# Kernel optimization log

Measured on AMD Instinct MI355X. Metric: run time of the kernel, lower is better.

The kernel has to match this reference:

```python
import jax, jax.numpy as jnp
import numpy as np
import math

N_NODES, N_EDGES, NNZ, D, L = 100000, 20000, 500000, 128, 4
ALPHA, LAMDA = 0.1, 0.5


def setup_inputs() -> dict:
    key = jax.random.key(0)
    ks = jax.random.split(key, 16)
    x = jax.random.normal(ks[0], (N_NODES, D), jnp.float32)
    e = jax.random.normal(ks[1], (N_EDGES, D), jnp.float32)
    nodes = jax.random.randint(ks[2], (NNZ,), 0, N_NODES)
    edges = jnp.sort(jax.random.randint(ks[3], (NNZ,), 0, N_EDGES)).at[-1].set(N_EDGES - 1)
    hyperedge_index = jnp.stack([nodes, edges]).astype(jnp.int32)
    dist_v2e = jax.random.randint(ks[4], (NNZ,), 0, 64).astype(jnp.float32)
    deg_v2e = jax.random.randint(ks[5], (NNZ,), 0, 64).astype(jnp.float32)
    dist_e2v = jax.random.randint(ks[6], (NNZ,), 0, 64).astype(jnp.float32)
    deg_e2v = jax.random.randint(ks[7], (NNZ,), 0, 64).astype(jnp.float32)
    s = 0.05
    W0 = jax.random.normal(ks[8], (D, D), jnp.float32) * s
    b0 = jnp.zeros((D,), jnp.float32)
    Wn = jax.random.normal(ks[9], (L, D, D), jnp.float32) * s
    We = jax.random.normal(ks[10], (L, D, D), jnp.float32) * s
    attn_w = jax.random.normal(ks[11], (L, 2 * D), jnp.float32) * s
    attn_b = jnp.zeros((L,), jnp.float32)
    wd_w = jax.random.normal(ks[12], (L,), jnp.float32) * s
    wd_b = jnp.zeros((L,), jnp.float32)
    wg_w = jax.random.normal(ks[13], (L,), jnp.float32) * s
    wg_b = jnp.zeros((L,), jnp.float32)
    return dict(x=x, e=e, hyperedge_index=hyperedge_index, dist_v2e=dist_v2e,
                deg_v2e=deg_v2e, dist_e2v=dist_e2v, deg_e2v=deg_e2v,
                W0=W0, b0=b0, Wn=Wn, We=We, attn_w=attn_w, attn_b=attn_b,
                wd_w=wd_w, wd_b=wd_b, wg_w=wg_w, wg_b=wg_b)


def _seg_softmax(s, idx, num):
    # numerically-stable scatter_softmax over segments idx
    m = jax.ops.segment_max(s, idx, num_segments=num)
    ex = jnp.exp(s - m[idx])
    den = jax.ops.segment_sum(ex, idx, num_segments=num)
    return ex / den[idx]


def _forward(x, e, hei, dv2e, gv2e, de2v, ge2v, W0, b0, Wn, We, aw, ab, wdw, wdb, wgw, wgb):
    nodes, edges = hei[0], hei[1]
    N, E = x.shape[0], e.shape[0]
    ones = jnp.ones(nodes.shape[0], x.dtype)
    dV = jax.ops.segment_sum(ones, nodes, num_segments=N)
    cnt = jax.ops.segment_sum(ones, edges, num_segments=E)
    dE = jax.ops.segment_sum(dV[nodes], edges, num_segments=E) / jnp.maximum(cnt, 1.0)
    degV = jnp.where(dV > 0, dV ** -0.5, 1.0)[:, None]   # [N,1]
    degE = jnp.where(dE > 0, dE ** -0.5, 1.0)[:, None]   # [E,1]

    x = jax.nn.relu(x @ W0 + b0)
    x0, e0 = x, e
    d = x.shape[1]
    for i in range(L):
        beta = math.log(LAMDA / (i + 1) + 1.0)
        # v2e attention: concat [x[nodes], e[edges]] -> softmax over edge segments
        sx1 = x @ aw[i, :d]; se1 = e @ aw[i, d:]
        s_v2e = sx1[nodes] + se1[edges] + ab[i] + dv2e * wdw[i] + wdb[i] + gv2e * wgw[i] + wgb[i]
        a_v2e = _seg_softmax(s_v2e, edges, E)[:, None]
        # e2v attention (flipped): concat [e[edges], x[nodes]] -> softmax over node segments
        se2 = e @ aw[i, :d]; sx2 = x @ aw[i, d:]
        s_e2v = se2[edges] + sx2[nodes] + ab[i] + de2v * wdw[i] + wdb[i] + ge2v * wgw[i] + wgb[i]
        a_e2v = _seg_softmax(s_e2v, nodes, N)[:, None]

        Xe1 = jax.ops.segment_sum(x[nodes] * a_v2e, edges, num_segments=E) * degE
        Xv1 = jax.ops.segment_sum(Xe1[edges] * a_e2v, nodes, num_segments=N) * degV
        Xv2 = jax.ops.segment_sum(e[edges] * a_e2v, nodes, num_segments=N) * degV
        Xe2 = jax.ops.segment_sum(Xv2[nodes] * a_v2e, edges, num_segments=E) * degE
        xm = (Xv1 + Xv2) * 0.5
        em = (Xe1 + Xe2) * 0.5
        xi = (1 - ALPHA) * xm + ALPHA * x0
        x = (1 - beta) * xi + beta * (xi @ Wn[i])
        ei = (1 - ALPHA) * em + ALPHA * e0
        e = (1 - beta) * ei + beta * (ei @ We[i])
        if i < L - 1:
            x = jax.nn.relu(x)
            e = jax.nn.relu(e)
    return x, e


def reference(x, e, hyperedge_index, dist_v2e, deg_v2e, dist_e2v, deg_e2v,
              W0, b0, Wn, We, attn_w, attn_b, wd_w, wd_b, wg_w, wg_b):
    return _forward(x, e, hyperedge_index, dist_v2e, deg_v2e, dist_e2v, deg_e2v,
                    W0, b0, Wn, We, attn_w, attn_b, wd_w, wd_b, wg_w, wg_b)
```

## Files before the change

kernel.cpp:

```cpp
#include <hip/hip_runtime.h>
#include <hip/hip_fp16.h>
#include <math.h>

#define DD 128
#define SCAN_BLOCKS 256
#define SMAX_CAP 128

typedef _Float16 f16x8 __attribute__((ext_vector_type(8)));
typedef float f32x4 __attribute__((ext_vector_type(4)));

__device__ inline float wave_sum(float v){
#pragma unroll
  for (int m = 32; m >= 1; m >>= 1) v += __shfl_xor(v, m, 64);
  return v;
}
__device__ inline int wave_sum_i(int v){
#pragma unroll
  for (int m = 32; m >= 1; m >>= 1) v += __shfl_xor(v, m, 64);
  return v;
}


__global__ void k_edge_offsets(const int* __restrict__ edges, int nnz, int E,
                               int* __restrict__ eo){
  int e = blockIdx.x * blockDim.x + threadIdx.x;
  if (e > E) return;
  int lo = 0, hi = nnz;
  while (lo < hi){ int mid = (lo + hi) >> 1; if (edges[mid] < e) lo = mid + 1; else hi = mid; }
  eo[e] = lo;
}

__global__ void k_hist(const int* __restrict__ nodes, int nnz, int* __restrict__ dV){
  int k = blockIdx.x * blockDim.x + threadIdx.x;
  if (k < nnz) atomicAdd(&dV[nodes[k]], 1);
}

__global__ __launch_bounds__(256) void k_scan_partial(const int* __restrict__ dV, int N,
                                                      int* __restrict__ part){
  int b = blockIdx.x, t = threadIdx.x;
  int chunk = (N + SCAN_BLOCKS - 1) / SCAN_BLOCKS;
  int s0 = b * chunk, s1 = min(s0 + chunk, N);
  int sum = 0;
  for (int n = s0 + t; n < s1; n += 256) sum += dV[n];
  sum = wave_sum_i(sum);
  __shared__ int wred[4];
  int lane = t & 63, wid = t >> 6;
  if (lane == 0) wred[wid] = sum;
  __syncthreads();
  if (t == 0) part[b] = wred[0] + wred[1] + wred[2] + wred[3];
}

__global__ __launch_bounds__(SCAN_BLOCKS) void k_scan_blocksums(int* __restrict__ part){
  __shared__ int sh[SCAN_BLOCKS];
  int t = threadIdx.x;
  int v = part[t];
  sh[t] = v; __syncthreads();
  for (int off = 1; off < SCAN_BLOCKS; off <<= 1){
    int add = (t >= off) ? sh[t - off] : 0;
    __syncthreads();
    sh[t] += add;
    __syncthreads();
  }
  part[t] = sh[t] - v;
}

__global__ __launch_bounds__(256) void k_scan_apply(const int* __restrict__ dV, int N, int nnz,
    const int* __restrict__ partScan, int* __restrict__ no, int* __restrict__ nfill,
    float* __restrict__ degV){
  int b = blockIdx.x, t = threadIdx.x;
  int chunk = (N + SCAN_BLOCKS - 1) / SCAN_BLOCKS;
  int s0 = b * chunk, s1 = min(s0 + chunk, N);
  int lane = t & 63, wid = t >> 6;
  __shared__ int wtot[4];
  __shared__ int s_run;
  if (t == 0) s_run = partScan[b];
  __syncthreads();
  for (int base = s0; base < s1; base += 256){
    int n = base + t;
    int d = (n < s1) ? dV[n] : 0;
    int v = d;
#pragma unroll
    for (int off = 1; off < 64; off <<= 1){
      int o = __shfl_up(v, off, 64);
      if (lane >= off) v += o;
    }
    if (lane == 63) wtot[wid] = v;
    __syncthreads();
    int run0 = s_run;
    int woff = 0;
    for (int w = 0; w < wid; w++) woff += wtot[w];
    if (n < s1){
      int excl = run0 + woff + v - d;
      no[n] = excl; nfill[n] = excl;
      degV[n] = d > 0 ? 1.0f / sqrtf((float)d) : 1.0f;
    }
    int btot = wtot[0] + wtot[1] + wtot[2] + wtot[3];
    __syncthreads();
    if (t == 0) s_run = run0 + btot;
    __syncthreads();
  }
  if (b == 0 && t == 0) no[N] = nnz;
}

__global__ void k_perm(const int* __restrict__ nodes, int nnz,
                       int* __restrict__ nfill, int* __restrict__ perm){
  int k = blockIdx.x * blockDim.x + threadIdx.x;
  if (k < nnz){ int pos = atomicAdd(&nfill[nodes[k]], 1); perm[pos] = k; }
}

__global__ void k_pack(const int* __restrict__ perm, const int* __restrict__ edges,
                       const float* __restrict__ dist, const float* __restrict__ deg,
                       int nnz, float2* __restrict__ pack){
  int j = blockIdx.x * blockDim.x + threadIdx.x;
  if (j < nnz){
    int k = perm[j];
    pack[j] = make_float2(__int_as_float(edges[k]), dist[k] + 64.f * deg[k]);
  }
}

__global__ void k_edge_deg(const int* __restrict__ nodes, const int* __restrict__ eo, int E,
                           const int* __restrict__ dV, float* __restrict__ degE){
  int e = blockIdx.x * blockDim.x + threadIdx.x;
  if (e >= E) return;
  int b = eo[e], en = eo[e + 1];
  float s = 0.f;
  for (int k = b; k < en; k++) s += (float)dV[nodes[k]];
  float cnt = (float)(en - b);
  float dE = s / fmaxf(cnt, 1.0f);
  degE[e] = dE > 0.f ? 1.0f / sqrtf(dE) : 1.0f;
}

__global__ __launch_bounds__(256) void k_einit(const float2* __restrict__ e_in2,
    const float* __restrict__ aw1, const float* __restrict__ aw2,
    int E, __half2* __restrict__ ET, __half2* __restrict__ e0h,
    float* __restrict__ se1, float* __restrict__ se2){
  int wave = threadIdx.x >> 6, lane = threadIdx.x & 63;
  int e = blockIdx.x * 4 + wave;
  if (e >= E) return;
  float2 v = e_in2[(size_t)e * 64 + lane];
  __half2 h = __floats2half2_rn(v.x, v.y);
  ET[(size_t)e * 128 + 2 * lane + 1] = h;
  e0h[(size_t)e * 64 + lane] = h;
  float2 a2v = ((const float2*)aw2)[lane];
  float2 a1v = ((const float2*)aw1)[lane];
  float s1 = v.x * a2v.x + v.y * a2v.y;
  float s2 = v.x * a1v.x + v.y * a1v.y;
  s1 = wave_sum(s1); s2 = wave_sum(s2);
  if (lane == 0){ se1[e] = s1; se2[e] = s2; }
}

__global__ void k_wcast(const float* __restrict__ W0, const float* __restrict__ Wn,
                        const float* __restrict__ We, _Float16* __restrict__ Wt){
  int idx = blockIdx.x * 256 + threadIdx.x;
  if (idx >= 9 * 16384) return;
  int m = idx >> 14, r = idx & 16383;
  int n = r >> 7, k = r & 127;
  float v;
  if (m == 0){
    v = W0[k * 128 + n];
  } else {
    int i = (m <= 4) ? m - 1 : m - 5;
    const float* src = (m <= 4) ? Wn + (size_t)i * 16384 : We + (size_t)i * 16384;
    float beta = logf(0.5f / (float)(i + 1) + 1.0f);
    v = beta * src[k * 128 + n] + ((n == k) ? (1.0f - beta) : 0.f);
  }
  Wt[(size_t)m * 16384 + n * 128 + k] = (_Float16)v;
}


__device__ inline void acc8h(const float4 q, float w, float* a){
  float2 h0 = __half22float2(*(const __half2*)&q.x);
  float2 h1 = __half22float2(*(const __half2*)&q.y);
  float2 h2v = __half22float2(*(const __half2*)&q.z);
  float2 h3 = __half22float2(*(const __half2*)&q.w);
  a[0] += w * h0.x; a[1] += w * h0.y; a[2] += w * h1.x; a[3] += w * h1.y;
  a[4] += w * h2v.x; a[5] += w * h2v.y; a[6] += w * h3.x; a[7] += w * h3.y;
}

__global__ __launch_bounds__(256) void k_sma1(
    const int* __restrict__ nodes, const int* __restrict__ eo,
    const float* __restrict__ sx1, const float* __restrict__ se1,
    const float* __restrict__ dist, const float* __restrict__ deg,
    const float* __restrict__ ab, const float* __restrict__ wdw, const float* __restrict__ wdb,
    const float* __restrict__ wgw, const float* __restrict__ wgb, int li,
    const float* __restrict__ degE, const float4* __restrict__ xh4,
    int E, float* __restrict__ a_v2e, float* __restrict__ esc, __half2* __restrict__ ET){
  __shared__ float lw[8][SMAX_CAP];
  int l32 = threadIdx.x & 31;
  int grp = threadIdx.x >> 5;
  int e = blockIdx.x * 8 + grp;
  if (e >= E) return;
  int b = eo[e], en = eo[e + 1];
  int l16 = l32 & 15, hf = l32 >> 4;
  if (b >= en){
    if (l32 == 0) esc[e] = 0.f;
    if (hf == 0){
      __half2 z = __floats2half2_rn(0.f, 0.f);
      size_t o = (size_t)e * 128 + 8 * l16;
      ET[o] = z; ET[o + 2] = z; ET[o + 4] = z; ET[o + 6] = z;
    }
    return;
  }
  float base = se1[e] + ab[li] + wdb[li] + wgb[li];
  float wd = wdw[li], wg = wgw[li];
  float m = -INFINITY;
  float sreg[4];
#pragma unroll
  for (int c = 0; c < 4; c++){
    int k = b + l32 + 32 * c;
    if (k < en){
      float s = sx1[nodes[k]] + base + dist[k] * wd + deg[k] * wg;
      sreg[c] = s; m = fmaxf(m, s);
    }
  }
  for (int k = b + l32 + SMAX_CAP; k < en; k += 32){
    float s = sx1[nodes[k]] + base + dist[k] * wd + deg[k] * wg;
    m = fmaxf(m, s);
  }
#pragma unroll
  for (int mm = 16; mm >= 1; mm >>= 1) m = fmaxf(m, __shfl_xor(m, mm, 32));
  float sum = 0.f;
#pragma unroll
  for (int c = 0; c < 4; c++){
    int k = b + l32 + 32 * c;
    if (k < en){
      float ex = __expf(sreg[c] - m);
      a_v2e[k] = ex; lw[grp][l32 + 32 * c] = ex; sum += ex;
    }
  }
  for (int k = b + l32 + SMAX_CAP; k < en; k += 32){
    float s = sx1[nodes[k]] + base + dist[k] * wd + deg[k] * wg;
    float ex = __expf(s - m);
    a_v2e[k] = ex; sum += ex;
  }
#pragma unroll
  for (int mm = 16; mm >= 1; mm >>= 1) sum += __shfl_xor(sum, mm, 32);
  float sc = degE[e] / sum;
  if (l32 == 0) esc[e] = sc;
  float a[8] = {0.f, 0.f, 0.f, 0.f, 0.f, 0.f, 0.f, 0.f};
  int k = b + hf;
  for (; k + 2 < en; k += 4){
    int n0 = nodes[k], n1 = nodes[k + 2];
    float w0 = (k - b < SMAX_CAP) ? lw[grp][k - b] : a_v2e[k];
    float w1 = (k + 2 - b < SMAX_CAP) ? lw[grp][k + 2 - b] : a_v2e[k + 2];
    float4 v0 = xh4[(size_t)n0 * 16 + l16];
    float4 v1 = xh4[(size_t)n1 * 16 + l16];
    acc8h(v0, w0, a); acc8h(v1, w1, a);
  }
  for (; k < en; k += 2){
    int n = nodes[k];
    float w = (k - b < SMAX_CAP) ? lw[grp][k - b] : a_v2e[k];
    float4 v = xh4[(size_t)n * 16 + l16];
    acc8h(v, w, a);
  }
#pragma unroll
  for (int j = 0; j < 8; j++) a[j] += __shfl_xor(a[j], 16, 32);
  if (hf == 0){
    size_t o = (size_t)e * 128 + 8 * l16;
    ET[o]     = __floats2half2_rn(a[0] * sc, a[1] * sc);
    ET[o + 2] = __floats2half2_rn(a[2] * sc, a[3] * sc);
    ET[o + 4] = __floats2half2_rn(a[4] * sc, a[5] * sc);
    ET[o + 6] = __floats2half2_rn(a[6] * sc, a[7] * sc);
  }
}

__device__ inline void acc8(const float4 q, float w, float* a1, float* a2){
  float2 x0 = __half22float2(*(const __half2*)&q.x);
  float2 e0 = __half22float2(*(const __half2*)&q.y);
  float2 x1 = __half22float2(*(const __half2*)&q.z);
  float2 e1 = __half22float2(*(const __half2*)&q.w);
  a1[0] += w * x0.x; a1[1] += w * x0.y; a1[2] += w * x1.x; a1[3] += w * x1.y;
  a2[0] += w * e0.x; a2[1] += w * e0.y; a2[2] += w * e1.x; a2[3] += w * e1.y;
}

__global__ __launch_bounds__(256) void k_agg2f(
    const float2* __restrict__ pack, const int* __restrict__ no,
    const float* __restrict__ se2, const float* __restrict__ sx2,
    const float* __restrict__ ab, const float* __restrict__ wdw, const float* __restrict__ wdb,
    const float* __restrict__ wgw, const float* __restrict__ wgb, int li,
    const float4* __restrict__ ETq,
    const float* __restrict__ degV, const __half2* __restrict__ x0h,
    int N, __half2* __restrict__ Xv2h, __half2* __restrict__ xiH){
  int l32 = threadIdx.x & 31;
  int grp = threadIdx.x >> 5;
  int n = blockIdx.x * 8 + grp;
  if (n >= N) return;
  int b = no[n], en = no[n + 1];
  float base = sx2[n] + ab[li] + wdb[li] + wgb[li];
  float wd = wdw[li], wg = wgw[li];
  float2 x0v2 = *(const float2*)&x0h[(size_t)n * 64 + 2 * l32];
  float l_run = 0.f;
  float a1[4] = {0.f, 0.f, 0.f, 0.f}, a2[4] = {0.f, 0.f, 0.f, 0.f};
  if (en - b <= 32){
    int cs = en - b;
    float s = -INFINITY; int e_l = 0;
    if (l32 < cs){
      float2 pk = pack[b + l32];
      e_l = __float_as_int(pk.x);
      int vi = (int)pk.y;
      s = se2[e_l] + base + (float)(vi & 63) * wd + (float)(vi >> 6) * wg;
    }
    float m_c = s;
#pragma unroll
    for (int mm = 16; mm >= 1; mm >>= 1) m_c = fmaxf(m_c, __shfl_xor(m_c, mm, 32));
    float p = (l32 < cs) ? __expf(s - m_c) : 0.f;
    l_run = p;
#pragma unroll
    for (int mm = 16; mm >= 1; mm >>= 1) l_run += __shfl_xor(l_run, mm, 32);
    int jj = 0;
    for (; jj + 3 < cs; jj += 4){
      float w0 = __shfl(p, jj, 32);
      float w1 = __shfl(p, jj + 1, 32);
      float w2 = __shfl(p, jj + 2, 32);
      float w3 = __shfl(p, jj + 3, 32);
      int e0i = __shfl(e_l, jj, 32);
      int e1i = __shfl(e_l, jj + 1, 32);
      int e2i = __shfl(e_l, jj + 2, 32);
      int e3i = __shfl(e_l, jj + 3, 32);
      float4 q0 = ETq[(size_t)e0i * 32 + l32];
      float4 q1 = ETq[(size_t)e1i * 32 + l32];
      float4 q2 = ETq[(size_t)e2i * 32 + l32];
      float4 q3 = ETq[(size_t)e3i * 32 + l32];
      acc8(q0, w0, a1, a2);
      acc8(q1, w1, a1, a2);
      acc8(q2, w2, a1, a2);
      acc8(q3, w3, a1, a2);
    }
    for (; jj < cs; jj++){
      float w = __shfl(p, jj, 32);
      int ei_ = __shfl(e_l, jj, 32);
      float4 q = ETq[(size_t)ei_ * 32 + l32];
      acc8(q, w, a1, a2);
    }
  } else {
    float m_run = -INFINITY;
    for (int cb = b; cb < en; cb += 32){
      int cs = min(32, en - cb);
      float s = -INFINITY; int e_l = 0;
      if (l32 < cs){
        float2 pk = pack[cb + l32];
        e_l = __float_as_int(pk.x);
        int vi = (int)pk.y;
        s = se2[e_l] + base + (float)(vi & 63) * wd + (float)(vi >> 6) * wg;
      }
      float m_c = s;
#pragma unroll
      for (int mm = 16; mm >= 1; mm >>= 1) m_c = fmaxf(m_c, __shfl_xor(m_c, mm, 32));
      float p = (l32 < cs) ? __expf(s - m_c) : 0.f;
      float l_c = p;
#pragma unroll
      for (int mm = 16; mm >= 1; mm >>= 1) l_c += __shfl_xor(l_c, mm, 32);
      float m_new = fmaxf(m_run, m_c);
      float f_old = __expf(m_run - m_new);
      float f_c = __expf(m_c - m_new);
#pragma unroll
      for (int r = 0; r < 4; r++){ a1[r] *= f_old; a2[r] *= f_old; }
      l_run = l_run * f_old + l_c * f_c;
      m_run = m_new;
      int jj = 0;
      for (; jj + 3 < cs; jj += 4){
        float w0 = __shfl(p, jj, 32) * f_c;
        float w1 = __shfl(p, jj + 1, 32) * f_c;
        float w2 = __shfl(p, jj + 2, 32) * f_c;
        float w3 = __shfl(p, jj + 3, 32) * f_c;
        int e0i = __shfl(e_l, jj, 32);
        int e1i = __shfl(e_l, jj + 1, 32);
        int e2i = __shfl(e_l, jj + 2, 32);
        int e3i = __shfl(e_l, jj + 3, 32);
        float4 q0 = ETq[(size_t)e0i * 32 + l32];
        float4 q1 = ETq[(size_t)e1i * 32 + l32];
        float4 q2 = ETq[(size_t)e2i * 32 + l32];
        float4 q3 = ETq[(size_t)e3i * 32 + l32];
        acc8(q0, w0, a1, a2);
        acc8(q1, w1, a1, a2);
        acc8(q2, w2, a1, a2);
        acc8(q3, w3, a1, a2);
      }
      for (; jj < cs; jj++){
        float w = __shfl(p, jj, 32) * f_c;
        int ei_ = __shfl(e_l, jj, 32);
        float4 q = ETq[(size_t)ei_ * 32 + l32];
        acc8(q, w, a1, a2);
      }
    }
  }
  float inv = l_run > 0.f ? 1.0f / l_run : 0.f;
  float dv = degV[n] * inv;
  float2 st;
  *(__half2*)&st.x = __floats2half2_rn(a2[0] * dv, a2[1] * dv);
  *(__half2*)&st.y = __floats2half2_rn(a2[2] * dv, a2[3] * dv);
  *(float2*)&Xv2h[(size_t)n * 64 + 2 * l32] = st;
  float2 h0 = __half22float2(*(const __half2*)&x0v2.x);
  float2 h1 = __half22float2(*(const __half2*)&x0v2.y);
  float2 xo;
  *(__half2*)&xo.x = __floats2half2_rn(0.45f * dv * (a1[0] + a2[0]) + 0.1f * h0.x,
                                       0.45f * dv * (a1[1] + a2[1]) + 0.1f * h0.y);
  *(__half2*)&xo.y = __floats2half2_rn(0.45f * dv * (a1[2] + a2[2]) + 0.1f * h1.x,
                                       0.45f * dv * (a1[3] + a2[3]) + 0.1f * h1.y);
  *(float2*)&xiH[(size_t)n * 64 + 2 * l32] = xo;
}

__global__ __launch_bounds__(256) void k_agg3(const int* __restrict__ nodes, const int* __restrict__ eo,
    const float4* __restrict__ Xv2h4, const float* __restrict__ a_v2e, const float* __restrict__ esc,
    const float4* __restrict__ ETq, const float4* __restrict__ e0h4,
    int E, __half2* __restrict__ eiH){
  int l32 = threadIdx.x & 31;
  int grp = threadIdx.x >> 5;
  int e = blockIdx.x * 8 + grp;
  if (e >= E) return;
  int b = eo[e], en = eo[e + 1];
  int l16 = l32 & 15, hf = l32 >> 4;
  float a[8] = {0.f, 0.f, 0.f, 0.f, 0.f, 0.f, 0.f, 0.f};
  int k = b + hf;
  for (; k + 2 < en; k += 4){
    int n0 = nodes[k], n1 = nodes[k + 2];
    float w0 = a_v2e[k], w1 = a_v2e[k + 2];
    float4 v0 = Xv2h4[(size_t)n0 * 16 + l16];
    float4 v1 = Xv2h4[(size_t)n1 * 16 + l16];
    acc8h(v0, w0, a); acc8h(v1, w1, a);
  }
  for (; k < en; k += 2){
    int n = nodes[k];
    float w = a_v2e[k];
    float4 v = Xv2h4[(size_t)n * 16 + l16];
    acc8h(v, w, a);
  }
#pragma unroll
  for (int j = 0; j < 8; j++) a[j] += __shfl_xor(a[j], 16, 32);
  if (hf == 0){
    float dE = esc[e];
    float4 q0 = ETq[(size_t)e * 32 + 2 * l16];
    float4 q1 = ETq[(size_t)e * 32 + 2 * l16 + 1];
    float2 x01 = __half22float2(*(const __half2*)&q0.x);
    float2 x23 = __half22float2(*(const __half2*)&q0.z);
    float2 x45 = __half22float2(*(const __half2*)&q1.x);
    float2 x67 = __half22float2(*(const __half2*)&q1.z);
    float4 ev = e0h4[(size_t)e * 16 + l16];
    float2 g0 = __half22float2(*(const __half2*)&ev.x);
    float2 g1 = __half22float2(*(const __half2*)&ev.y);
    float2 g2 = __half22float2(*(const __half2*)&ev.z);
    float2 g3 = __half22float2(*(const __half2*)&ev.w);
    float4 o;
    *(__half2*)&o.x = __floats2half2_rn(0.45f * (x01.x + a[0] * dE) + 0.1f * g0.x,
                                        0.45f * (x01.y + a[1] * dE) + 0.1f * g0.y);
    *(__half2*)&o.y = __floats2half2_rn(0.45f * (x23.x + a[2] * dE) + 0.1f * g1.x,
                                        0.45f * (x23.y + a[3] * dE) + 0.1f * g1.y);
    *(__half2*)&o.z = __floats2half2_rn(0.45f * (x45.x + a[4] * dE) + 0.1f * g2.x,
                                        0.45f * (x45.y + a[5] * dE) + 0.1f * g2.y);
    *(__half2*)&o.w = __floats2half2_rn(0.45f * (x67.x + a[6] * dE) + 0.1f * g3.x,
                                        0.45f * (x67.y + a[7] * dE) + 0.1f * g3.y);
    *(float4*)&eiH[(size_t)e * 64 + 4 * l16] = o;
  }
}

__device__ __forceinline__ void gemm_body(
    const _Float16* __restrict__ Ah, const _Float16* __restrict__ Wt,
    float* __restrict__ outf, _Float16* __restrict__ outh, int et,
    const float* __restrict__ awA, const float* __restrict__ awB,
    float* __restrict__ sA, float* __restrict__ sB,
    int nrows, int do_relu, int row0){
  int lane = threadIdx.x & 63;
  int lm = lane & 15;
  int lk8 = (lane >> 4) * 8;
  int arow = row0 + lm; if (arow >= nrows) arow = nrows - 1;
  f16x8 afrag[4];
#pragma unroll
  for (int ks = 0; ks < 4; ks++)
    afrag[ks] = *(const f16x8*)(Ah + (size_t)arow * 128 + ks * 32 + lk8);
  int rbase = (lane >> 4) * 4;
  float da[4] = {0.f, 0.f, 0.f, 0.f}, db[4] = {0.f, 0.f, 0.f, 0.f};
  for (int t = 0; t < 8; t++){
    f32x4 acc = {0.f, 0.f, 0.f, 0.f};
#pragma unroll
    for (int ks = 0; ks < 4; ks++){
      f16x8 bf = *(const f16x8*)(Wt + (size_t)(t * 16 + lm) * 128 + ks * 32 + lk8);
      acc = __builtin_amdgcn_mfma_f32_16x16x32_f16(afrag[ks], bf, acc, 0, 0, 0);
    }
    int col = t * 16 + lm;
    float wa = 0.f, wb = 0.f;
    if (awA){ wa = awA[col]; wb = awB[col]; }
#pragma unroll
    for (int r = 0; r < 4; r++){
      int gr = row0 + rbase + r;
      if (gr >= nrows) continue;
      float v = acc[r];
      if (do_relu) v = fmaxf(v, 0.f);
      if (outf) outf[(size_t)gr * 128 + col] = v;
      if (outh){
        if (et) outh[(size_t)gr * 256 + (col >> 1) * 4 + 2 + (col & 1)] = (_Float16)v;
        else    outh[(size_t)gr * 128 + col] = (_Float16)v;
      }
      da[r] += v * wa; db[r] += v * wb;
    }
  }
  if (awA){
#pragma unroll
    for (int r = 0; r < 4; r++){
      float a = da[r], bb = db[r];
#pragma unroll
      for (int m = 8; m >= 1; m >>= 1){
        a += __shfl_xor(a, m, 64);
        bb += __shfl_xor(bb, m, 64);
      }
      int gr = row0 + rbase + r;
      if (lm == 0 && gr < nrows){ sA[gr] = a; sB[gr] = bb; }
    }
  }
}

__global__ __launch_bounds__(256) void k_gemm2(
    const _Float16* __restrict__ Ax, const _Float16* __restrict__ Wx,
    const _Float16* __restrict__ Ae, const _Float16* __restrict__ Wte,
    float* __restrict__ outfx, _Float16* __restrict__ outhx,
    float* __restrict__ outfe, _Float16* __restrict__ outhe,
    const float* __restrict__ awAx, const float* __restrict__ awBx,
    float* __restrict__ sAx, float* __restrict__ sBx,
    const float* __restrict__ awAe, const float* __restrict__ awBe,
    float* __restrict__ sAe, float* __restrict__ sBe,
    int nrx, int nre, int nbx, int do_relu){
  int wave = threadIdx.x >> 6;
  if ((int)blockIdx.x < nbx){
    int row0 = blockIdx.x * 64 + wave * 16;
    if (row0 >= nrx) return;
    gemm_body(Ax, Wx, outfx, outhx, 0, awAx, awBx, sAx, sBx, nrx, do_relu, row0);
  } else {
    int row0 = (blockIdx.x - nbx) * 64 + wave * 16;
    if (row0 >= nre) return;
    gemm_body(Ae, Wte, outfe, outhe, 1, awAe, awBe, sAe, sBe, nre, do_relu, row0);
  }
}

__global__ __launch_bounds__(256) void k_gemm0(
    const float* __restrict__ Af, const _Float16* __restrict__ Wt,
    const float* __restrict__ bias,
    _Float16* __restrict__ outh, _Float16* __restrict__ outh2,
    const float* __restrict__ awA, const float* __restrict__ awB,
    float* __restrict__ sA, float* __restrict__ sB, int nrows){
  int wave = threadIdx.x >> 6, lane = threadIdx.x & 63;
  int row0 = blockIdx.x * 64 + wave * 16;
  if (row0 >= nrows) return;
  int lm = lane & 15;
  int lk8 = (lane >> 4) * 8;
  int arow = row0 + lm; if (arow >= nrows) arow = nrows - 1;
  const float* ap = Af + (size_t)arow * 128;
  f16x8 afrag[4];
#pragma unroll
  for (int ks = 0; ks < 4; ks++){
    float4 v0 = *(const float4*)(ap + ks * 32 + lk8);
    float4 v1 = *(const float4*)(ap + ks * 32 + lk8 + 4);
    f16x8 a;
    a[0] = (_Float16)v0.x; a[1] = (_Float16)v0.y; a[2] = (_Float16)v0.z; a[3] = (_Float16)v0.w;
    a[4] = (_Float16)v1.x; a[5] = (_Float16)v1.y; a[6] = (_Float16)v1.z; a[7] = (_Float16)v1.w;
    afrag[ks] = a;
  }
  int rbase = (lane >> 4) * 4;
  float da[4] = {0.f, 0.f, 0.f, 0.f}, db[4] = {0.f, 0.f, 0.f, 0.f};
  for (int t = 0; t < 8; t++){
    f32x4 acc = {0.f, 0.f, 0.f, 0.f};
#pragma unroll
    for (int ks = 0; ks < 4; ks++){
      f16x8 bf = *(const f16x8*)(Wt + (size_t)(t * 16 + lm) * 128 + ks * 32 + lk8);
      acc = __builtin_amdgcn_mfma_f32_16x16x32_f16(afrag[ks], bf, acc, 0, 0, 0);
    }
    int col = t * 16 + lm;
    float wa = awA[col], wb = awB[col];
    float bi = bias[col];
#pragma unroll
    for (int r = 0; r < 4; r++){
      int gr = row0 + rbase + r;
      if (gr >= nrows) continue;
      float v = fmaxf(acc[r] + bi, 0.f);
      outh[(size_t)gr * 128 + col] = (_Float16)v;
      outh2[(size_t)gr * 128 + col] = (_Float16)v;
      da[r] += v * wa; db[r] += v * wb;
    }
  }
#pragma unroll
  for (int r = 0; r < 4; r++){
    float a = da[r], bb = db[r];
#pragma unroll
    for (int m = 8; m >= 1; m >>= 1){
      a += __shfl_xor(a, m, 64);
      bb += __shfl_xor(bb, m, 64);
    }
    int gr = row0 + rbase + r;
    if (lm == 0 && gr < nrows){ sA[gr] = a; sB[gr] = bb; }
  }
}


extern "C" void kernel_launch(void* const* d_in, const int* in_sizes, int n_in,
                              void* d_out, int out_size, void* d_ws, size_t ws_size,
                              hipStream_t stream) {
  const float* x_in     = (const float*)d_in[0];
  const float* e_in     = (const float*)d_in[1];
  const int*   hei      = (const int*)d_in[2];
  const float* dist_v2e = (const float*)d_in[3];
  const float* deg_v2e  = (const float*)d_in[4];
  const float* dist_e2v = (const float*)d_in[5];
  const float* deg_e2v  = (const float*)d_in[6];
  const float* W0       = (const float*)d_in[7];
  const float* b0       = (const float*)d_in[8];
  const float* Wn       = (const float*)d_in[9];
  const float* We       = (const float*)d_in[10];
  const float* attn_w   = (const float*)d_in[11];
  const float* attn_b   = (const float*)d_in[12];
  const float* wd_w     = (const float*)d_in[13];
  const float* wd_b     = (const float*)d_in[14];
  const float* wg_w     = (const float*)d_in[15];
  const float* wg_b     = (const float*)d_in[16];

  const int N   = in_sizes[0] / DD;
  const int E   = in_sizes[1] / DD;
  const int NNZ = in_sizes[2] / 2;
  const int* nodesArr = hei;
  const int* edgesArr = hei + NNZ;

  float* out_x = (float*)d_out;
  float* out_e = (float*)d_out + (size_t)N * DD;

  __half2* Xv2h = (__half2*)out_x;
  __half2* xh   = (__half2*)((char*)out_x + (size_t)N * DD * 2);
  __half2* ET   = (__half2*)out_e;
  const float4* ETq = (const float4*)out_e;

  char* wsp = (char*)d_ws;
  auto alloc = [&](size_t bytes) -> void* {
    void* p = (void*)wsp;
    wsp += (bytes + 255) / 256 * 256;
    return p;
  };
  _Float16* x0h  = (_Float16*)alloc((size_t)N * DD * 2);
  _Float16* xiH  = (_Float16*)alloc((size_t)N * DD * 2);
  _Float16* eiH  = (_Float16*)alloc((size_t)E * DD * 2);
  _Float16* e0h  = (_Float16*)alloc((size_t)E * DD * 2);
  _Float16* Wt   = (_Float16*)alloc((size_t)9 * 16384 * 2);
  float* sx1   = (float*)alloc((size_t)N * 4);
  float* sx2   = (float*)alloc((size_t)N * 4);
  float* se1   = (float*)alloc((size_t)E * 4);
  float* se2   = (float*)alloc((size_t)E * 4);
  float* a_v2e = (float*)alloc((size_t)NNZ * 4);
  float* degV  = (float*)alloc((size_t)N * 4);
  float* degE  = (float*)alloc((size_t)E * 4);
  float* esc   = (float*)alloc((size_t)E * 4);
  float2* pack = (float2*)alloc((size_t)NNZ * 8);
  int* dV_i  = (int*)alloc((size_t)N * 4);
  int* no_   = (int*)alloc((size_t)(N + 1) * 4);
  int* nfill = (int*)alloc((size_t)N * 4);
  int* perm  = (int*)alloc((size_t)NNZ * 4);
  int* eo    = (int*)alloc((size_t)(E + 1) * 4);
  int* part  = (int*)alloc((size_t)SCAN_BLOCKS * 4);

  hipMemsetAsync(dV_i, 0, (size_t)N * 4, stream);
  k_edge_offsets<<<(E + 1 + 255) / 256, 256, 0, stream>>>(edgesArr, NNZ, E, eo);
  k_hist<<<(NNZ + 255) / 256, 256, 0, stream>>>(nodesArr, NNZ, dV_i);
  k_scan_partial<<<SCAN_BLOCKS, 256, 0, stream>>>(dV_i, N, part);
  k_scan_blocksums<<<1, SCAN_BLOCKS, 0, stream>>>(part);
  k_scan_apply<<<SCAN_BLOCKS, 256, 0, stream>>>(dV_i, N, NNZ, part, no_, nfill, degV);
  k_perm<<<(NNZ + 255) / 256, 256, 0, stream>>>(nodesArr, NNZ, nfill, perm);
  k_pack<<<(NNZ + 255) / 256, 256, 0, stream>>>(perm, edgesArr, dist_e2v, deg_e2v, NNZ, pack);
  k_edge_deg<<<(E + 255) / 256, 256, 0, stream>>>(nodesArr, eo, E, dV_i, degE);
  k_wcast<<<(9 * 16384 + 255) / 256, 256, 0, stream>>>(W0, Wn, We, Wt);

  const float* aw1_0 = attn_w;
  const float* aw2_0 = attn_w + 128;

  k_einit<<<(E + 3) / 4, 256, 0, stream>>>((const float2*)e_in, aw1_0, aw2_0,
                                            E, ET, (__half2*)e0h, se1, se2);

  k_gemm0<<<(N + 63) / 64, 256, 0, stream>>>(x_in, Wt, b0,
      (_Float16*)xh, x0h, aw1_0, aw2_0, sx1, sx2, N);

  const int nbx = (N + 63) / 64, nbe = (E + 63) / 64;
  for (int i = 0; i < 4; i++){
    const float* aw1n = (i < 3) ? attn_w + (size_t)(i + 1) * 256        : nullptr;
    const float* aw2n = (i < 3) ? attn_w + (size_t)(i + 1) * 256 + 128  : nullptr;

    k_sma1<<<(E + 7) / 8, 256, 0, stream>>>(nodesArr, eo, sx1, se1,
        dist_v2e, deg_v2e, attn_b, wd_w, wd_b, wg_w, wg_b, i, degE,
        (const float4*)xh, E, a_v2e, esc, ET);

    k_agg2f<<<(N + 7) / 8, 256, 0, stream>>>(pack, no_, se2, sx2,
        attn_b, wd_w, wd_b, wg_w, wg_b, i,
        ETq, degV, (const __half2*)x0h, N, Xv2h, (__half2*)xiH);
    k_agg3<<<(E + 7) / 8, 256, 0, stream>>>(nodesArr, eo, (const float4*)Xv2h,
        a_v2e, esc, ETq, (const float4*)e0h, E, (__half2*)eiH);

    k_gemm2<<<nbx + nbe, 256, 0, stream>>>(
        xiH, Wt + (size_t)(1 + i) * 16384,
        eiH, Wt + (size_t)(5 + i) * 16384,
        (i == 3) ? out_x : nullptr, (i < 3) ? (_Float16*)xh : nullptr,
        (i == 3) ? out_e : nullptr, (i < 3) ? (_Float16*)ET : nullptr,
        aw1n, aw2n, sx1, sx2,
        aw2n, aw1n, se1, se2,
        N, E, nbx, i < 3 ? 1 : 0);
  }
}
```

Measured before the change: 844.8 us.

## Fuse node GEMM into edge aggregation launch, merge perm/pack, unroll gather by 8

Node-side GEMM blocks are appended to the edge-aggregation kernel so both run in one launch and can overlap, while the edge GEMM moves to its own kernel that runs after. The perm and pack kernels are merged into one that scatters straight into the packed array, which removes the intermediate perm buffer. The short-segment gather loop in agg2f is unrolled to 8 loads in flight. Xv2h moves from the output buffer to its own workspace allocation, since the node GEMM now writes xh into the output buffer while agg3 is still reading Xv2h.

```diff
diff --git a/kernel.cpp b/kernel.cpp
--- a/kernel.cpp
+++ b/kernel.cpp
@@ -102,19 +102,13 @@
   if (b == 0 && t == 0) no[N] = nnz;
 }
 
-__global__ void k_perm(const int* __restrict__ nodes, int nnz,
-                       int* __restrict__ nfill, int* __restrict__ perm){
+__global__ void k_permpack(const int* __restrict__ nodes, const int* __restrict__ edges,
+                           const float* __restrict__ dist, const float* __restrict__ deg,
+                           int nnz, int* __restrict__ nfill, float2* __restrict__ pack){
   int k = blockIdx.x * blockDim.x + threadIdx.x;
-  if (k < nnz){ int pos = atomicAdd(&nfill[nodes[k]], 1); perm[pos] = k; }
-}
-
-__global__ void k_pack(const int* __restrict__ perm, const int* __restrict__ edges,
-                       const float* __restrict__ dist, const float* __restrict__ deg,
-                       int nnz, float2* __restrict__ pack){
-  int j = blockIdx.x * blockDim.x + threadIdx.x;
-  if (j < nnz){
-    int k = perm[j];
-    pack[j] = make_float2(__int_as_float(edges[k]), dist[k] + 64.f * deg[k]);
+  if (k < nnz){
+    int pos = atomicAdd(&nfill[nodes[k]], 1);
+    pack[pos] = make_float2(__int_as_float(edges[k]), dist[k] + 64.f * deg[k]);
   }
 }
 
@@ -308,23 +302,29 @@
 #pragma unroll
     for (int mm = 16; mm >= 1; mm >>= 1) l_run += __shfl_xor(l_run, mm, 32);
     int jj = 0;
+    for (; jj + 7 < cs; jj += 8){
+      float w[8]; int ei[8]; float4 q[8];
+#pragma unroll
+      for (int u = 0; u < 8; u++){
+        w[u] = __shfl(p, jj + u, 32);
+        ei[u] = __shfl(e_l, jj + u, 32);
+      }
+#pragma unroll
+      for (int u = 0; u < 8; u++) q[u] = ETq[(size_t)ei[u] * 32 + l32];
+#pragma unroll
+      for (int u = 0; u < 8; u++) acc8(q[u], w[u], a1, a2);
+    }
     for (; jj + 3 < cs; jj += 4){
-      float w0 = __shfl(p, jj, 32);
-      float w1 = __shfl(p, jj + 1, 32);
-      float w2 = __shfl(p, jj + 2, 32);
-      float w3 = __shfl(p, jj + 3, 32);
-      int e0i = __shfl(e_l, jj, 32);
-      int e1i = __shfl(e_l, jj + 1, 32);
-      int e2i = __shfl(e_l, jj + 2, 32);
-      int e3i = __shfl(e_l, jj + 3, 32);
-      float4 q0 = ETq[(size_t)e0i * 32 + l32];
-      float4 q1 = ETq[(size_t)e1i * 32 + l32];
-      float4 q2 = ETq[(size_t)e2i * 32 + l32];
-      float4 q3 = ETq[(size_t)e3i * 32 + l32];
-      acc8(q0, w0, a1, a2);
-      acc8(q1, w1, a1, a2);
-      acc8(q2, w2, a1, a2);
-      acc8(q3, w3, a1, a2);
+      float w[4]; int ei[4]; float4 q[4];
+#pragma unroll
+      for (int u = 0; u < 4; u++){
+        w[u] = __shfl(p, jj + u, 32);
+        ei[u] = __shfl(e_l, jj + u, 32);
+      }
+#pragma unroll
+      for (int u = 0; u < 4; u++) q[u] = ETq[(size_t)ei[u] * 32 + l32];
+#pragma unroll
+      for (int u = 0; u < 4; u++) acc8(q[u], w[u], a1, a2);
     }
     for (; jj < cs; jj++){
       float w = __shfl(p, jj, 32);
@@ -400,10 +400,77 @@
   *(float2*)&xiH[(size_t)n * 64 + 2 * l32] = xo;
 }
 
-__global__ __launch_bounds__(256) void k_agg3(const int* __restrict__ nodes, const int* __restrict__ eo,
-    const float4* __restrict__ Xv2h4, const float* __restrict__ a_v2e, const float* __restrict__ esc,
+__device__ __forceinline__ void gemm_body(
+    const _Float16* __restrict__ Ah, const _Float16* __restrict__ Wt,
+    float* __restrict__ outf, _Float16* __restrict__ outh, int et,
+    const float* __restrict__ awA, const float* __restrict__ awB,
+    float* __restrict__ sA, float* __restrict__ sB,
+    int nrows, int do_relu, int row0){
+  int lane = threadIdx.x & 63;
+  int lm = lane & 15;
+  int lk8 = (lane >> 4) * 8;
+  int arow = row0 + lm; if (arow >= nrows) arow = nrows - 1;
+  f16x8 afrag[4];
+#pragma unroll
+  for (int ks = 0; ks < 4; ks++)
+    afrag[ks] = *(const f16x8*)(Ah + (size_t)arow * 128 + ks * 32 + lk8);
+  int rbase = (lane >> 4) * 4;
+  float da[4] = {0.f, 0.f, 0.f, 0.f}, db[4] = {0.f, 0.f, 0.f, 0.f};
+  for (int t = 0; t < 8; t++){
+    f32x4 acc = {0.f, 0.f, 0.f, 0.f};
+#pragma unroll
+    for (int ks = 0; ks < 4; ks++){
+      f16x8 bf = *(const f16x8*)(Wt + (size_t)(t * 16 + lm) * 128 + ks * 32 + lk8);
+      acc = __builtin_amdgcn_mfma_f32_16x16x32_f16(afrag[ks], bf, acc, 0, 0, 0);
+    }
+    int col = t * 16 + lm;
+    float wa = 0.f, wb = 0.f;
+    if (awA){ wa = awA[col]; wb = awB[col]; }
+#pragma unroll
+    for (int r = 0; r < 4; r++){
+      int gr = row0 + rbase + r;
+      if (gr >= nrows) continue;
+      float v = acc[r];
+      if (do_relu) v = fmaxf(v, 0.f);
+      if (outf) outf[(size_t)gr * 128 + col] = v;
+      if (outh){
+        if (et) outh[(size_t)gr * 256 + (col >> 1) * 4 + 2 + (col & 1)] = (_Float16)v;
+        else    outh[(size_t)gr * 128 + col] = (_Float16)v;
+      }
+      da[r] += v * wa; db[r] += v * wb;
+    }
+  }
+  if (awA){
+#pragma unroll
+    for (int r = 0; r < 4; r++){
+      float a = da[r], bb = db[r];
+#pragma unroll
+      for (int m = 8; m >= 1; m >>= 1){
+        a += __shfl_xor(a, m, 64);
+        bb += __shfl_xor(bb, m, 64);
+      }
+      int gr = row0 + rbase + r;
+      if (lm == 0 && gr < nrows){ sA[gr] = a; sB[gr] = bb; }
+    }
+  }
+}
+
+__global__ __launch_bounds__(256) void k_a3gx(
+    const int* __restrict__ nodes, const int* __restrict__ eo,
+    const float4* __restrict__ Xv2h4, const float* __restrict__ a_v2e,
+    const float* __restrict__ esc,
     const float4* __restrict__ ETq, const float4* __restrict__ e0h4,
-    int E, __half2* __restrict__ eiH){
+    int E, __half2* __restrict__ eiH, int nbA,
+    const _Float16* __restrict__ Ah, const _Float16* __restrict__ Wt,
+    float* __restrict__ outf, _Float16* __restrict__ outh,
+    const float* __restrict__ awA, const float* __restrict__ awB,
+    float* __restrict__ sA, float* __restrict__ sB, int N, int do_relu){
+  if ((int)blockIdx.x >= nbA){
+    int row0 = (blockIdx.x - nbA) * 64 + (threadIdx.x >> 6) * 16;
+    if (row0 >= N) return;
+    gemm_body(Ah, Wt, outf, outh, 0, awA, awB, sA, sB, N, do_relu, row0);
+    return;
+  }
   int l32 = threadIdx.x & 31;
   int grp = threadIdx.x >> 5;
   int e = blockIdx.x * 8 + grp;
@@ -453,81 +520,14 @@
   }
 }
 
-__device__ __forceinline__ void gemm_body(
+__global__ __launch_bounds__(256) void k_gemme(
     const _Float16* __restrict__ Ah, const _Float16* __restrict__ Wt,
-    float* __restrict__ outf, _Float16* __restrict__ outh, int et,
+    float* __restrict__ outf, _Float16* __restrict__ outh,
     const float* __restrict__ awA, const float* __restrict__ awB,
-    float* __restrict__ sA, float* __restrict__ sB,
-    int nrows, int do_relu, int row0){
-  int lane = threadIdx.x & 63;
-  int lm = lane & 15;
-  int lk8 = (lane >> 4) * 8;
-  int arow = row0 + lm; if (arow >= nrows) arow = nrows - 1;
-  f16x8 afrag[4];
-#pragma unroll
-  for (int ks = 0; ks < 4; ks++)
-    afrag[ks] = *(const f16x8*)(Ah + (size_t)arow * 128 + ks * 32 + lk8);
-  int rbase = (lane >> 4) * 4;
-  float da[4] = {0.f, 0.f, 0.f, 0.f}, db[4] = {0.f, 0.f, 0.f, 0.f};
-  for (int t = 0; t < 8; t++){
-    f32x4 acc = {0.f, 0.f, 0.f, 0.f};
-#pragma unroll
-    for (int ks = 0; ks < 4; ks++){
-      f16x8 bf = *(const f16x8*)(Wt + (size_t)(t * 16 + lm) * 128 + ks * 32 + lk8);
-      acc = __builtin_amdgcn_mfma_f32_16x16x32_f16(afrag[ks], bf, acc, 0, 0, 0);
-    }
-    int col = t * 16 + lm;
-    float wa = 0.f, wb = 0.f;
-    if (awA){ wa = awA[col]; wb = awB[col]; }
-#pragma unroll
-    for (int r = 0; r < 4; r++){
-      int gr = row0 + rbase + r;
-      if (gr >= nrows) continue;
-      float v = acc[r];
-      if (do_relu) v = fmaxf(v, 0.f);
-      if (outf) outf[(size_t)gr * 128 + col] = v;
-      if (outh){
-        if (et) outh[(size_t)gr * 256 + (col >> 1) * 4 + 2 + (col & 1)] = (_Float16)v;
-        else    outh[(size_t)gr * 128 + col] = (_Float16)v;
-      }
-      da[r] += v * wa; db[r] += v * wb;
-    }
-  }
-  if (awA){
-#pragma unroll
-    for (int r = 0; r < 4; r++){
-      float a = da[r], bb = db[r];
-#pragma unroll
-      for (int m = 8; m >= 1; m >>= 1){
-        a += __shfl_xor(a, m, 64);
-        bb += __shfl_xor(bb, m, 64);
-      }
-      int gr = row0 + rbase + r;
-      if (lm == 0 && gr < nrows){ sA[gr] = a; sB[gr] = bb; }
-    }
-  }
-}
-
-__global__ __launch_bounds__(256) void k_gemm2(
-    const _Float16* __restrict__ Ax, const _Float16* __restrict__ Wx,
-    const _Float16* __restrict__ Ae, const _Float16* __restrict__ Wte,
-    float* __restrict__ outfx, _Float16* __restrict__ outhx,
-    float* __restrict__ outfe, _Float16* __restrict__ outhe,
-    const float* __restrict__ awAx, const float* __restrict__ awBx,
-    float* __restrict__ sAx, float* __restrict__ sBx,
-    const float* __restrict__ awAe, const float* __restrict__ awBe,
-    float* __restrict__ sAe, float* __restrict__ sBe,
-    int nrx, int nre, int nbx, int do_relu){
-  int wave = threadIdx.x >> 6;
-  if ((int)blockIdx.x < nbx){
-    int row0 = blockIdx.x * 64 + wave * 16;
-    if (row0 >= nrx) return;
-    gemm_body(Ax, Wx, outfx, outhx, 0, awAx, awBx, sAx, sBx, nrx, do_relu, row0);
-  } else {
-    int row0 = (blockIdx.x - nbx) * 64 + wave * 16;
-    if (row0 >= nre) return;
-    gemm_body(Ae, Wte, outfe, outhe, 1, awAe, awBe, sAe, sBe, nre, do_relu, row0);
-  }
+    float* __restrict__ sA, float* __restrict__ sB, int nrows, int do_relu){
+  int row0 = blockIdx.x * 64 + (threadIdx.x >> 6) * 16;
+  if (row0 >= nrows) return;
+  gemm_body(Ah, Wt, outf, outh, 1, awA, awB, sA, sB, nrows, do_relu, row0);
 }
 
 __global__ __launch_bounds__(256) void k_gemm0(
@@ -619,7 +619,6 @@
   float* out_x = (float*)d_out;
   float* out_e = (float*)d_out + (size_t)N * DD;
 
-  __half2* Xv2h = (__half2*)out_x;
   __half2* xh   = (__half2*)((char*)out_x + (size_t)N * DD * 2);
   __half2* ET   = (__half2*)out_e;
   const float4* ETq = (const float4*)out_e;
@@ -631,6 +630,7 @@
     return p;
   };
   _Float16* x0h  = (_Float16*)alloc((size_t)N * DD * 2);
+  _Float16* Xv2h = (_Float16*)alloc((size_t)N * DD * 2);
   _Float16* xiH  = (_Float16*)alloc((size_t)N * DD * 2);
   _Float16* eiH  = (_Float16*)alloc((size_t)E * DD * 2);
   _Float16* e0h  = (_Float16*)alloc((size_t)E * DD * 2);
@@ -647,7 +647,6 @@
   int* dV_i  = (int*)alloc((size_t)N * 4);
   int* no_   = (int*)alloc((size_t)(N + 1) * 4);
   int* nfill = (int*)alloc((size_t)N * 4);
-  int* perm  = (int*)alloc((size_t)NNZ * 4);
   int* eo    = (int*)alloc((size_t)(E + 1) * 4);
   int* part  = (int*)alloc((size_t)SCAN_BLOCKS * 4);
 
@@ -657,8 +656,8 @@
   k_scan_partial<<<SCAN_BLOCKS, 256, 0, stream>>>(dV_i, N, part);
   k_scan_blocksums<<<1, SCAN_BLOCKS, 0, stream>>>(part);
   k_scan_apply<<<SCAN_BLOCKS, 256, 0, stream>>>(dV_i, N, NNZ, part, no_, nfill, degV);
-  k_perm<<<(NNZ + 255) / 256, 256, 0, stream>>>(nodesArr, NNZ, nfill, perm);
-  k_pack<<<(NNZ + 255) / 256, 256, 0, stream>>>(perm, edgesArr, dist_e2v, deg_e2v, NNZ, pack);
+  k_permpack<<<(NNZ + 255) / 256, 256, 0, stream>>>(nodesArr, edgesArr, dist_e2v, deg_e2v,
+                                                    NNZ, nfill, pack);
   k_edge_deg<<<(E + 255) / 256, 256, 0, stream>>>(nodesArr, eo, E, dV_i, degE);
   k_wcast<<<(9 * 16384 + 255) / 256, 256, 0, stream>>>(W0, Wn, We, Wt);
 
@@ -671,7 +670,7 @@
   k_gemm0<<<(N + 63) / 64, 256, 0, stream>>>(x_in, Wt, b0,
       (_Float16*)xh, x0h, aw1_0, aw2_0, sx1, sx2, N);
 
-  const int nbx = (N + 63) / 64, nbe = (E + 63) / 64;
+  const int nbA = (E + 7) / 8, nbG = (N + 63) / 64;
   for (int i = 0; i < 4; i++){
     const float* aw1n = (i < 3) ? attn_w + (size_t)(i + 1) * 256        : nullptr;
     const float* aw2n = (i < 3) ? attn_w + (size_t)(i + 1) * 256 + 128  : nullptr;
@@ -682,17 +681,17 @@
 
     k_agg2f<<<(N + 7) / 8, 256, 0, stream>>>(pack, no_, se2, sx2,
         attn_b, wd_w, wd_b, wg_w, wg_b, i,
-        ETq, degV, (const __half2*)x0h, N, Xv2h, (__half2*)xiH);
-    k_agg3<<<(E + 7) / 8, 256, 0, stream>>>(nodesArr, eo, (const float4*)Xv2h,
-        a_v2e, esc, ETq, (const float4*)e0h, E, (__half2*)eiH);
-
-    k_gemm2<<<nbx + nbe, 256, 0, stream>>>(
+        ETq, degV, (const __half2*)x0h, N, (__half2*)Xv2h, (__half2*)xiH);
+
+    k_a3gx<<<nbA + nbG, 256, 0, stream>>>(
+        nodesArr, eo, (const float4*)Xv2h, a_v2e, esc, ETq, (const float4*)e0h,
+        E, (__half2*)eiH, nbA,
         xiH, Wt + (size_t)(1 + i) * 16384,
-        eiH, Wt + (size_t)(5 + i) * 16384,
         (i == 3) ? out_x : nullptr, (i < 3) ? (_Float16*)xh : nullptr,
+        aw1n, aw2n, sx1, sx2, N, i < 3 ? 1 : 0);
+
+    k_gemme<<<(E + 63) / 64, 256, 0, stream>>>(eiH, Wt + (size_t)(5 + i) * 16384,
         (i == 3) ? out_e : nullptr, (i < 3) ? (_Float16*)ET : nullptr,
-        aw1n, aw2n, sx1, sx2,
-        aw2n, aw1n, se1, se2,
-        N, E, nbx, i < 3 ? 1 : 0);
-  }
-}
+        aw2n, aw1n, se1, se2, E, i < 3 ? 1 : 0);
+  }
+}
```

Measured after the change: 864.8 us. +2.4%, slower.
